# Kernel tuning notes

Measured on AMD Instinct MI355X. Metric: run time of the kernel, lower is better.

## Reference

```python
import jax, jax.numpy as jnp
import numpy as np

EMBED_DIM = 2048
NUM_HEADS = 16
HEAD_DIM = EMBED_DIM // NUM_HEADS
ROPE_BASE = 10000.0


def setup_inputs() -> dict:
    key = jax.random.key(0)
    ks = jax.random.split(key, 5)
    s = 1.0 / np.sqrt(EMBED_DIM)
    return {
        "x": jax.random.normal(ks[0], (2, 2048, EMBED_DIM), dtype=jnp.float32),
        "Wq": jax.random.normal(ks[1], (EMBED_DIM, EMBED_DIM), dtype=jnp.float32) * s,
        "Wk": jax.random.normal(ks[2], (EMBED_DIM, EMBED_DIM), dtype=jnp.float32) * s,
        "Wv": jax.random.normal(ks[3], (EMBED_DIM, EMBED_DIM), dtype=jnp.float32) * s,
        "Wo": jax.random.normal(ks[4], (EMBED_DIM, EMBED_DIM), dtype=jnp.float32) * s,
    }


def _rope(x):
    # x: [b, h, s, d]; standard rotate-half RoPE
    b, h, s, d = x.shape
    inv_freq = 1.0 / (ROPE_BASE ** (jnp.arange(0, d, 2, dtype=jnp.float32) / d))
    ang = jnp.arange(s, dtype=jnp.float32)[:, None] * inv_freq[None, :]  # [s, d/2]
    cos = jnp.concatenate([jnp.cos(ang), jnp.cos(ang)], axis=-1)  # [s, d]
    sin = jnp.concatenate([jnp.sin(ang), jnp.sin(ang)], axis=-1)
    x1, x2 = x[..., : d // 2], x[..., d // 2 :]
    rot = jnp.concatenate([-x2, x1], axis=-1)
    return x * cos + rot * sin


def reference(x, Wq, Wk, Wv, Wo):
    b, s, e = x.shape
    h, d = NUM_HEADS, HEAD_DIM
    # projections (torch Linear: x @ W.T); W here stored so that y = x @ W
    q = (x @ Wq).reshape(b, s, h, d).transpose(0, 2, 1, 3)
    k = (x @ Wk).reshape(b, s, h, d).transpose(0, 2, 1, 3)
    v = (x @ Wv).reshape(b, s, h, d).transpose(0, 2, 1, 3)
    q = _rope(q)
    k = _rope(k)
    att = jnp.einsum("bhqd,bhkd->bhqk", q, k) / jnp.sqrt(jnp.float32(d))
    causal = jnp.tril(jnp.ones((s, s), dtype=bool))
    att = jnp.where(causal, att, -jnp.inf)
    att = jax.nn.softmax(att, axis=-1)
    out = jnp.einsum("bhqk,bhkd->bhqd", att, v)
    out = out.transpose(0, 2, 1, 3).reshape(b, s, e)
    return out @ Wo
```

## Files before the change

kernel.cpp:

```cpp
#include <hip/hip_runtime.h>
#include <stdint.h>

#define EDIM 2048
#define HH 16
#define DD 128
#define SS 2048
#define BB 2

typedef __attribute__((ext_vector_type(8))) __bf16 bf16x8;
typedef __attribute__((ext_vector_type(8))) unsigned short ushort8;
typedef __attribute__((ext_vector_type(4))) unsigned short ushort4v;
typedef __attribute__((ext_vector_type(4))) float f32x4;

__device__ __forceinline__ unsigned short f2b(float f) {
    union { float f; unsigned int u; } v; v.f = f;
    unsigned int u = v.u;
    unsigned int r = (u + 0x7fffu + ((u >> 16) & 1u)) >> 16;
    return (unsigned short)r;
}
__device__ __forceinline__ float b2f(unsigned short h) {
    union { unsigned int u; float f; } v; v.u = ((unsigned int)h) << 16;
    return v.f;
}
__device__ __forceinline__ bf16x8 lds8(const unsigned short* p) {
    return __builtin_bit_cast(bf16x8, *(const ushort8*)p);
}
__device__ __forceinline__ void gl_lds16(const unsigned short* g, unsigned short* l) {
    __builtin_amdgcn_global_load_lds(
        (const __attribute__((address_space(1))) void*)(const void*)g,
        (__attribute__((address_space(3))) void*)(void*)l, 16, 0, 0);
}


__global__ __launch_bounds__(256) void k_cvt_x(const float4* __restrict__ x,
                                               ushort4v* __restrict__ xb) {
    size_t i = (size_t)blockIdx.x * 256 + threadIdx.x;
    float4 v = x[i];
    ushort4v o;
    o.x = f2b(v.x); o.y = f2b(v.y); o.z = f2b(v.z); o.w = f2b(v.w);
    xb[i] = o;
}

__global__ __launch_bounds__(256) void k_trans(const float* __restrict__ W0,
                                               const float* __restrict__ W1,
                                               const float* __restrict__ W2,
                                               const float* __restrict__ W3,
                                               unsigned short* __restrict__ Wt) {
    const float* W = (blockIdx.z == 0) ? W0 : (blockIdx.z == 1) ? W1
                     : (blockIdx.z == 2) ? W2 : W3;
    unsigned short* out = Wt + (size_t)blockIdx.z * EDIM * EDIM;
    __shared__ float t[64][65];
    int r0 = blockIdx.y * 64, c0 = blockIdx.x * 64;
#pragma unroll
    for (int i = 0; i < 16; ++i) {
        int e = threadIdx.x + i * 256; int r = e >> 6, c = e & 63;
        t[r][c] = W[(size_t)(r0 + r) * EDIM + c0 + c];
    }
    __syncthreads();
#pragma unroll
    for (int i = 0; i < 16; ++i) {
        int e = threadIdx.x + i * 256; int r = e >> 6, c = e & 63;
        out[(size_t)(c0 + r) * EDIM + r0 + c] = f2b(t[c][r]);
    }
}


__device__ __forceinline__ void gemm_core(const unsigned short* __restrict__ A,
                                          const unsigned short* __restrict__ Bt,
                                          int K, size_t m0, size_t n0,
                                          unsigned short* As, unsigned short* Bs,
                                          f32x4 acc[4][4], int wave, int lane) {
    const int wm = wave >> 1, wn = wave & 1;
    const int lg = lane >> 4, lr = lane & 15;
    for (int kt = 0; kt < K; kt += 32) {
#pragma unroll
        for (int j = 0; j < 2; ++j) {
            const int cb = j * 256 + wave * 64;
            const int c  = cb + lane;
            gl_lds16(A  + (m0 + (size_t)(c >> 2)) * K + kt + (c & 3) * 8, As + cb * 8);
            gl_lds16(Bt + (n0 + (size_t)(c >> 2)) * K + kt + (c & 3) * 8, Bs + cb * 8);
        }
        __syncthreads();
        bf16x8 af[4], bg[4];
#pragma unroll
        for (int i = 0; i < 4; ++i) {
            af[i] = lds8(As + (wm * 64 + i * 16 + lr) * 32 + lg * 8);
            bg[i] = lds8(Bs + (wn * 64 + i * 16 + lr) * 32 + lg * 8);
        }
#pragma unroll
        for (int i = 0; i < 4; ++i)
#pragma unroll
            for (int j = 0; j < 4; ++j)
                acc[i][j] = __builtin_amdgcn_mfma_f32_16x16x32_bf16(af[i], bg[j], acc[i][j], 0, 0, 0);
        __syncthreads();
    }
}

__global__ __launch_bounds__(256) void k_gemm_qkv(const unsigned short* __restrict__ xb,
                                                  const unsigned short* __restrict__ Wt,
                                                  unsigned short* __restrict__ Qd,
                                                  unsigned short* __restrict__ Kd,
                                                  unsigned short* __restrict__ Vtd) {
    __shared__ alignas(16) unsigned short As[128 * 32];
    __shared__ alignas(16) unsigned short Bs[128 * 32];
    const int tid = threadIdx.x, wave = tid >> 6, lane = tid & 63;
    const int wsel = blockIdx.y >> 4;
    const size_t m0 = (size_t)blockIdx.x * 128;
    const size_t n0 = (size_t)(blockIdx.y & 15) * 128;
    const unsigned short* Bw = Wt + (size_t)wsel * EDIM * EDIM;
    f32x4 acc[4][4] = {};
    gemm_core(xb, Bw, EDIM, m0, n0, As, Bs, acc, wave, lane);
    const int wm = wave >> 1, wn = wave & 1, lg = lane >> 4, lr = lane & 15;
    if (wsel < 2) {
        unsigned short* dst = wsel ? Kd : Qd;
#pragma unroll
        for (int i = 0; i < 4; ++i)
#pragma unroll
            for (int j = 0; j < 4; ++j)
#pragma unroll
                for (int r = 0; r < 4; ++r) {
                    int row = (int)m0 + wm * 64 + i * 16 + lg * 4 + r;
                    int e   = (int)n0 + wn * 64 + j * 16 + lr;
                    int b = row >> 11, s = row & (SS - 1);
                    int h = e >> 7,  d = e & (DD - 1);
                    dst[(((size_t)(b * HH + h)) * SS + s) * DD + d] = f2b(acc[i][j][r]);
                }
    } else {
#pragma unroll
        for (int i = 0; i < 4; ++i)
#pragma unroll
            for (int j = 0; j < 4; ++j) {
                int row0 = (int)m0 + wm * 64 + i * 16 + lg * 4;
                int e    = (int)n0 + wn * 64 + j * 16 + lr;
                int b = row0 >> 11, s0 = row0 & (SS - 1);
                int h = e >> 7, d = e & (DD - 1);
                ushort4v pk;
                pk.x = f2b(acc[i][j][0]); pk.y = f2b(acc[i][j][1]);
                pk.z = f2b(acc[i][j][2]); pk.w = f2b(acc[i][j][3]);
                *(ushort4v*)(Vtd + (((size_t)(b * HH + h)) * DD + d) * SS + s0) = pk;
            }
    }
}

__global__ __launch_bounds__(256) void k_gemm_out(const unsigned short* __restrict__ Ob,
                                                  const unsigned short* __restrict__ Wto,
                                                  float* __restrict__ y) {
    __shared__ alignas(16) unsigned short As[128 * 32];
    __shared__ alignas(16) unsigned short Bs[128 * 32];
    const int tid = threadIdx.x, wave = tid >> 6, lane = tid & 63;
    const size_t m0 = (size_t)blockIdx.x * 128;
    const size_t n0 = (size_t)blockIdx.y * 128;
    f32x4 acc[4][4] = {};
    gemm_core(Ob, Wto, EDIM, m0, n0, As, Bs, acc, wave, lane);
    const int wm = wave >> 1, wn = wave & 1, lg = lane >> 4, lr = lane & 15;
#pragma unroll
    for (int i = 0; i < 4; ++i)
#pragma unroll
        for (int j = 0; j < 4; ++j)
#pragma unroll
            for (int r = 0; r < 4; ++r) {
                size_t row = m0 + wm * 64 + i * 16 + lg * 4 + r;
                size_t col = n0 + wn * 64 + j * 16 + lr;
                y[row * EDIM + col] = acc[i][j][r];
            }
}


__global__ __launch_bounds__(256) void k_rope(unsigned short* __restrict__ Q,
                                              unsigned short* __restrict__ K) {
    int idx = blockIdx.x * 256 + threadIdx.x;
    int i  = idx & 63;
    int s  = (idx >> 6) & (SS - 1);
    int bh = idx >> 17;
    size_t base = ((size_t)bh * SS + s) * DD;
    float inv = __expf(-0.14391156608f * (float)i);
    float ang = (float)s * inv;
    float sn, cs; sincosf(ang, &sn, &cs);
    const float qs = 0.08838834764831845f;
    float q1 = b2f(Q[base + i]), q2 = b2f(Q[base + 64 + i]);
    float k1 = b2f(K[base + i]), k2 = b2f(K[base + 64 + i]);
    Q[base + i]      = f2b((q1 * cs - q2 * sn) * qs);
    Q[base + 64 + i] = f2b((q2 * cs + q1 * sn) * qs);
    K[base + i]      = f2b(k1 * cs - k2 * sn);
    K[base + 64 + i] = f2b(k2 * cs + k1 * sn);
}


__global__ __launch_bounds__(256) void k_attn(const unsigned short* __restrict__ Q,
                                              const unsigned short* __restrict__ Kg,
                                              const unsigned short* __restrict__ Vt,
                                              unsigned short* __restrict__ Ob) {
    __shared__ alignas(16) unsigned short Ks[64 * 136];
    __shared__ alignas(16) unsigned short Vs[128 * 72];
    __shared__ alignas(16) unsigned short Ps[64 * 72];
    const int tid = threadIdx.x, wave = tid >> 6, lane = tid & 63;
    const int lg = lane >> 4, lr = lane & 15;
    const int bh = blockIdx.y;
    const int q0 = ((int)gridDim.x - 1 - (int)blockIdx.x) * 64;
    const size_t qkb = (size_t)bh * SS * DD;
    const size_t vbb = (size_t)bh * DD * SS;

    bf16x8 qf[4];
    {
        const unsigned short* qp = Q + qkb + (size_t)(q0 + wave * 16 + lr) * DD + lg * 8;
#pragma unroll
        for (int kk = 0; kk < 4; ++kk)
            qf[kk] = __builtin_bit_cast(bf16x8, *(const ushort8*)(qp + kk * 32));
    }
    f32x4 o[8] = {};
    float mrow[4], lrow[4];
#pragma unroll
    for (int r = 0; r < 4; ++r) { mrow[r] = -1e30f; lrow[r] = 0.f; }

    const int nt = q0 / 64 + 1;
    for (int t = 0; t < nt; ++t) {
        const int kv0 = t * 64;
        __syncthreads();
#pragma unroll
        for (int it = 0; it < 4; ++it) {
            int c = tid + it * 256;
            { int r = c >> 4, off = (c & 15) * 8;
              *(ushort8*)(Ks + r * 136 + off) =
                  *(const ushort8*)(Kg + qkb + (size_t)(kv0 + r) * DD + off); }
            { int dr = c >> 3, off = (c & 7) * 8;
              *(ushort8*)(Vs + dr * 72 + off) =
                  *(const ushort8*)(Vt + vbb + (size_t)dr * SS + kv0 + off); }
        }
        __syncthreads();

        f32x4 sa[4] = {};
#pragma unroll
        for (int nf = 0; nf < 4; ++nf)
#pragma unroll
            for (int kk = 0; kk < 4; ++kk) {
                bf16x8 kb = lds8(Ks + (nf * 16 + lr) * 136 + kk * 32 + lg * 8);
                sa[nf] = __builtin_amdgcn_mfma_f32_16x16x32_bf16(qf[kk], kb, sa[nf], 0, 0, 0);
            }
        if (t == nt - 1) {
#pragma unroll
            for (int nf = 0; nf < 4; ++nf)
#pragma unroll
                for (int r = 0; r < 4; ++r) {
                    int col = nf * 16 + lr, rw = wave * 16 + lg * 4 + r;
                    if (col > rw) sa[nf][r] = -__builtin_inff();
                }
        }
        float corr[4];
#pragma unroll
        for (int r = 0; r < 4; ++r) {
            float tm = fmaxf(fmaxf(sa[0][r], sa[1][r]), fmaxf(sa[2][r], sa[3][r]));
#pragma unroll
            for (int mm = 1; mm < 16; mm <<= 1) tm = fmaxf(tm, __shfl_xor(tm, mm));
            float mn = fmaxf(mrow[r], tm);
            corr[r] = __expf(mrow[r] - mn);
            mrow[r] = mn;
        }
#pragma unroll
        for (int nf = 0; nf < 4; ++nf)
#pragma unroll
            for (int r = 0; r < 4; ++r) {
                float p = __expf(sa[nf][r] - mrow[r]);
                sa[nf][r] = p;
                Ps[(wave * 16 + lg * 4 + r) * 72 + nf * 16 + lr] = f2b(p);
            }
#pragma unroll
        for (int r = 0; r < 4; ++r) {
            float sm = sa[0][r] + sa[1][r] + sa[2][r] + sa[3][r];
#pragma unroll
            for (int mm = 1; mm < 16; mm <<= 1) sm += __shfl_xor(sm, mm);
            lrow[r] = lrow[r] * corr[r] + sm;
        }
#pragma unroll
        for (int nf = 0; nf < 8; ++nf)
#pragma unroll
            for (int r = 0; r < 4; ++r) o[nf][r] *= corr[r];

        bf16x8 pa0 = lds8(Ps + (wave * 16 + lr) * 72 + lg * 8);
        bf16x8 pa1 = lds8(Ps + (wave * 16 + lr) * 72 + 32 + lg * 8);
#pragma unroll
        for (int nf = 0; nf < 8; ++nf) {
            bf16x8 v0 = lds8(Vs + (nf * 16 + lr) * 72 + lg * 8);
            bf16x8 v1 = lds8(Vs + (nf * 16 + lr) * 72 + 32 + lg * 8);
            o[nf] = __builtin_amdgcn_mfma_f32_16x16x32_bf16(pa0, v0, o[nf], 0, 0, 0);
            o[nf] = __builtin_amdgcn_mfma_f32_16x16x32_bf16(pa1, v1, o[nf], 0, 0, 0);
        }
    }
    const int b = bh >> 4, h = bh & 15;
#pragma unroll
    for (int nf = 0; nf < 8; ++nf)
#pragma unroll
        for (int r = 0; r < 4; ++r) {
            int s = q0 + wave * 16 + lg * 4 + r;
            int e = h * DD + nf * 16 + lr;
            Ob[((size_t)b * SS + s) * EDIM + e] = f2b(o[nf][r] / lrow[r]);
        }
}


extern "C" void kernel_launch(void* const* d_in, const int* in_sizes, int n_in,
                              void* d_out, int out_size, void* d_ws, size_t ws_size,
                              hipStream_t stream) {
    const float* x  = (const float*)d_in[0];
    const float* Wq = (const float*)d_in[1];
    const float* Wk = (const float*)d_in[2];
    const float* Wv = (const float*)d_in[3];
    const float* Wo = (const float*)d_in[4];
    float* y = (float*)d_out;
    char* ws = (char*)d_ws;
    unsigned short* xb  = (unsigned short*)(ws);
    unsigned short* Wt  = (unsigned short*)(ws + (size_t)16777216);
    unsigned short* Qd  = (unsigned short*)(ws + (size_t)50331648);
    unsigned short* Kd  = (unsigned short*)(ws + (size_t)67108864);
    unsigned short* Vtd = (unsigned short*)(ws + (size_t)83886080);
    unsigned short* Ob  = (unsigned short*)(ws + (size_t)100663296);

    hipLaunchKernelGGL(k_cvt_x, dim3(8192), dim3(256), 0, stream, (const float4*)x, (ushort4v*)xb);
    hipLaunchKernelGGL(k_trans, dim3(32, 32, 4), dim3(256), 0, stream, Wq, Wk, Wv, Wo, Wt);
    hipLaunchKernelGGL(k_gemm_qkv, dim3(32, 48), dim3(256), 0, stream, xb, Wt, Qd, Kd, Vtd);
    hipLaunchKernelGGL(k_rope, dim3(16384), dim3(256), 0, stream, Qd, Kd);
    hipLaunchKernelGGL(k_attn, dim3(32, 32), dim3(256), 0, stream, Qd, Kd, Vtd, Ob);
    hipLaunchKernelGGL(k_gemm_out, dim3(32, 16), dim3(256), 0, stream,
                       Ob, Wt + (size_t)3 * EDIM * EDIM, y);
}
```

Baseline: 509.1 us.

## Pair causal query tiles per block and restructure attention softmax pipeline

Each attention block now handles two query tiles (tp and 31-tp), which balances causal work and lets both share each staged K/V tile, halving the grid. K/V global loads are register-prefetched one tile ahead, the softmax uses exp2 with log2e folded into the Q scale, and rescaling is skipped unless the row max grows by more than 8. The row sum comes from an extra ones-row in V computed by MFMA instead of shuffles, and s_setprio is raised around MFMA sections. In exchange register pressure and LDS use rise, and the grid has fewer blocks.

```diff
diff --git a/kernel.cpp b/kernel.cpp
--- a/kernel.cpp
+++ b/kernel.cpp
@@ -176,7 +176,7 @@
     float inv = __expf(-0.14391156608f * (float)i);
     float ang = (float)s * inv;
     float sn, cs; sincosf(ang, &sn, &cs);
-    const float qs = 0.08838834764831845f;
+    const float qs = 0.08838834764831845f * 1.44269504088896340736f;
     float q1 = b2f(Q[base + i]), q2 = b2f(Q[base + 64 + i]);
     float k1 = b2f(K[base + i]), k2 = b2f(K[base + 64 + i]);
     Q[base + i]      = f2b((q1 * cs - q2 * sn) * qs);
@@ -186,113 +186,146 @@
 }
 
 
+__device__ __forceinline__ void attn_tile(const unsigned short* Ks, const unsigned short* Vs,
+                                          unsigned short* Ps, const bf16x8 qf[4],
+                                          f32x4 o[9], float mrow[4], bool maskdiag,
+                                          int wave, int lg, int lr) {
+    f32x4 sa[4] = {};
+    __builtin_amdgcn_s_setprio(1);
+#pragma unroll
+    for (int nf = 0; nf < 4; ++nf)
+#pragma unroll
+        for (int kk = 0; kk < 4; ++kk) {
+            bf16x8 kb = lds8(Ks + (nf * 16 + lr) * 136 + kk * 32 + lg * 8);
+            sa[nf] = __builtin_amdgcn_mfma_f32_16x16x32_bf16(qf[kk], kb, sa[nf], 0, 0, 0);
+        }
+    __builtin_amdgcn_s_setprio(0);
+    if (maskdiag) {
+#pragma unroll
+        for (int nf = 0; nf < 4; ++nf)
+#pragma unroll
+            for (int r = 0; r < 4; ++r) {
+                int col = nf * 16 + lr, rw = wave * 16 + lg * 4 + r;
+                if (col > rw) sa[nf][r] = -__builtin_inff();
+            }
+    }
+    float tm[4]; bool need = false;
+#pragma unroll
+    for (int r = 0; r < 4; ++r) {
+        float t = fmaxf(fmaxf(sa[0][r], sa[1][r]), fmaxf(sa[2][r], sa[3][r]));
+#pragma unroll
+        for (int mm = 1; mm < 16; mm <<= 1) t = fmaxf(t, __shfl_xor(t, mm));
+        tm[r] = t;
+        need = need || (t > mrow[r] + 8.0f);
+    }
+    if (__any(need)) {
+        float corr[4];
+#pragma unroll
+        for (int r = 0; r < 4; ++r) {
+            float mn = fmaxf(mrow[r], tm[r]);
+            corr[r] = exp2f(mrow[r] - mn);
+            mrow[r] = mn;
+        }
+#pragma unroll
+        for (int nf = 0; nf < 9; ++nf)
+#pragma unroll
+            for (int r = 0; r < 4; ++r) o[nf][r] *= corr[r];
+    }
+#pragma unroll
+    for (int nf = 0; nf < 4; ++nf)
+#pragma unroll
+        for (int r = 0; r < 4; ++r)
+            Ps[(wave * 16 + lg * 4 + r) * 72 + nf * 16 + lr] = f2b(exp2f(sa[nf][r] - mrow[r]));
+    bf16x8 pa0 = lds8(Ps + (wave * 16 + lr) * 72 + lg * 8);
+    bf16x8 pa1 = lds8(Ps + (wave * 16 + lr) * 72 + 32 + lg * 8);
+    __builtin_amdgcn_s_setprio(1);
+#pragma unroll
+    for (int nf = 0; nf < 9; ++nf) {
+        bf16x8 v0 = lds8(Vs + (nf * 16 + lr) * 72 + lg * 8);
+        bf16x8 v1 = lds8(Vs + (nf * 16 + lr) * 72 + 32 + lg * 8);
+        o[nf] = __builtin_amdgcn_mfma_f32_16x16x32_bf16(pa0, v0, o[nf], 0, 0, 0);
+        o[nf] = __builtin_amdgcn_mfma_f32_16x16x32_bf16(pa1, v1, o[nf], 0, 0, 0);
+    }
+    __builtin_amdgcn_s_setprio(0);
+}
+
 __global__ __launch_bounds__(256) void k_attn(const unsigned short* __restrict__ Q,
                                               const unsigned short* __restrict__ Kg,
                                               const unsigned short* __restrict__ Vt,
                                               unsigned short* __restrict__ Ob) {
     __shared__ alignas(16) unsigned short Ks[64 * 136];
-    __shared__ alignas(16) unsigned short Vs[128 * 72];
+    __shared__ alignas(16) unsigned short Vs[144 * 72];
     __shared__ alignas(16) unsigned short Ps[64 * 72];
     const int tid = threadIdx.x, wave = tid >> 6, lane = tid & 63;
     const int lg = lane >> 4, lr = lane & 15;
     const int bh = blockIdx.y;
-    const int q0 = ((int)gridDim.x - 1 - (int)blockIdx.x) * 64;
+    const int tp = blockIdx.x;
+    const int qa0 = tp * 64, qb0 = (31 - tp) * 64;
+    const int nta = tp + 1, ntb = 32 - tp;
     const size_t qkb = (size_t)bh * SS * DD;
     const size_t vbb = (size_t)bh * DD * SS;
 
-    bf16x8 qf[4];
     {
-        const unsigned short* qp = Q + qkb + (size_t)(q0 + wave * 16 + lr) * DD + lg * 8;
-#pragma unroll
-        for (int kk = 0; kk < 4; ++kk)
-            qf[kk] = __builtin_bit_cast(bf16x8, *(const ushort8*)(qp + kk * 32));
-    }
-    f32x4 o[8] = {};
-    float mrow[4], lrow[4];
-#pragma unroll
-    for (int r = 0; r < 4; ++r) { mrow[r] = -1e30f; lrow[r] = 0.f; }
-
-    const int nt = q0 / 64 + 1;
-    for (int t = 0; t < nt; ++t) {
-        const int kv0 = t * 64;
+        ushort4v one4; one4.x = 0x3F80; one4.y = 0x3F80; one4.z = 0x3F80; one4.w = 0x3F80;
+        *(ushort4v*)(Vs + (128 + (tid >> 4)) * 72 + (tid & 15) * 4) = one4;
+    }
+
+    bf16x8 qfA[4], qfB[4];
+    {
+        const unsigned short* qpA = Q + qkb + (size_t)(qa0 + wave * 16 + lr) * DD + lg * 8;
+        const unsigned short* qpB = Q + qkb + (size_t)(qb0 + wave * 16 + lr) * DD + lg * 8;
+#pragma unroll
+        for (int kk = 0; kk < 4; ++kk) {
+            qfA[kk] = __builtin_bit_cast(bf16x8, *(const ushort8*)(qpA + kk * 32));
+            qfB[kk] = __builtin_bit_cast(bf16x8, *(const ushort8*)(qpB + kk * 32));
+        }
+    }
+    f32x4 oA[9] = {}, oB[9] = {};
+    float mA[4], mB[4];
+#pragma unroll
+    for (int r = 0; r < 4; ++r) { mA[r] = -3e38f; mB[r] = -3e38f; }
+
+    ushort8 kr[4], vr[4];
+#pragma unroll
+    for (int i = 0; i < 4; ++i) {
+        int c = tid + i * 256;
+        kr[i] = *(const ushort8*)(Kg + qkb + (size_t)(c >> 4) * DD + (c & 15) * 8);
+        vr[i] = *(const ushort8*)(Vt + vbb + (size_t)(c >> 3) * SS + (c & 7) * 8);
+    }
+
+    for (int t = 0; t < ntb; ++t) {
         __syncthreads();
 #pragma unroll
-        for (int it = 0; it < 4; ++it) {
-            int c = tid + it * 256;
-            { int r = c >> 4, off = (c & 15) * 8;
-              *(ushort8*)(Ks + r * 136 + off) =
-                  *(const ushort8*)(Kg + qkb + (size_t)(kv0 + r) * DD + off); }
-            { int dr = c >> 3, off = (c & 7) * 8;
-              *(ushort8*)(Vs + dr * 72 + off) =
-                  *(const ushort8*)(Vt + vbb + (size_t)dr * SS + kv0 + off); }
+        for (int i = 0; i < 4; ++i) {
+            int c = tid + i * 256;
+            *(ushort8*)(Ks + (c >> 4) * 136 + (c & 15) * 8) = kr[i];
+            *(ushort8*)(Vs + (c >> 3) * 72 + (c & 7) * 8) = vr[i];
         }
         __syncthreads();
-
-        f32x4 sa[4] = {};
-#pragma unroll
-        for (int nf = 0; nf < 4; ++nf)
-#pragma unroll
-            for (int kk = 0; kk < 4; ++kk) {
-                bf16x8 kb = lds8(Ks + (nf * 16 + lr) * 136 + kk * 32 + lg * 8);
-                sa[nf] = __builtin_amdgcn_mfma_f32_16x16x32_bf16(qf[kk], kb, sa[nf], 0, 0, 0);
+        if (t + 1 < ntb) {
+            int kv0 = (t + 1) * 64;
+#pragma unroll
+            for (int i = 0; i < 4; ++i) {
+                int c = tid + i * 256;
+                kr[i] = *(const ushort8*)(Kg + qkb + (size_t)(kv0 + (c >> 4)) * DD + (c & 15) * 8);
+                vr[i] = *(const ushort8*)(Vt + vbb + (size_t)(c >> 3) * SS + kv0 + (c & 7) * 8);
             }
-        if (t == nt - 1) {
-#pragma unroll
-            for (int nf = 0; nf < 4; ++nf)
-#pragma unroll
-                for (int r = 0; r < 4; ++r) {
-                    int col = nf * 16 + lr, rw = wave * 16 + lg * 4 + r;
-                    if (col > rw) sa[nf][r] = -__builtin_inff();
-                }
-        }
-        float corr[4];
+        }
+        attn_tile(Ks, Vs, Ps, qfB, oB, mB, t == ntb - 1, wave, lg, lr);
+        if (t < nta)
+            attn_tile(Ks, Vs, Ps, qfA, oA, mA, t == nta - 1, wave, lg, lr);
+    }
+
+    const int b = bh >> 4, h = bh & 15;
+#pragma unroll
+    for (int nf = 0; nf < 8; ++nf)
 #pragma unroll
         for (int r = 0; r < 4; ++r) {
-            float tm = fmaxf(fmaxf(sa[0][r], sa[1][r]), fmaxf(sa[2][r], sa[3][r]));
-#pragma unroll
-            for (int mm = 1; mm < 16; mm <<= 1) tm = fmaxf(tm, __shfl_xor(tm, mm));
-            float mn = fmaxf(mrow[r], tm);
-            corr[r] = __expf(mrow[r] - mn);
-            mrow[r] = mn;
-        }
-#pragma unroll
-        for (int nf = 0; nf < 4; ++nf)
-#pragma unroll
-            for (int r = 0; r < 4; ++r) {
-                float p = __expf(sa[nf][r] - mrow[r]);
-                sa[nf][r] = p;
-                Ps[(wave * 16 + lg * 4 + r) * 72 + nf * 16 + lr] = f2b(p);
-            }
-#pragma unroll
-        for (int r = 0; r < 4; ++r) {
-            float sm = sa[0][r] + sa[1][r] + sa[2][r] + sa[3][r];
-#pragma unroll
-            for (int mm = 1; mm < 16; mm <<= 1) sm += __shfl_xor(sm, mm);
-            lrow[r] = lrow[r] * corr[r] + sm;
-        }
-#pragma unroll
-        for (int nf = 0; nf < 8; ++nf)
-#pragma unroll
-            for (int r = 0; r < 4; ++r) o[nf][r] *= corr[r];
-
-        bf16x8 pa0 = lds8(Ps + (wave * 16 + lr) * 72 + lg * 8);
-        bf16x8 pa1 = lds8(Ps + (wave * 16 + lr) * 72 + 32 + lg * 8);
-#pragma unroll
-        for (int nf = 0; nf < 8; ++nf) {
-            bf16x8 v0 = lds8(Vs + (nf * 16 + lr) * 72 + lg * 8);
-            bf16x8 v1 = lds8(Vs + (nf * 16 + lr) * 72 + 32 + lg * 8);
-            o[nf] = __builtin_amdgcn_mfma_f32_16x16x32_bf16(pa0, v0, o[nf], 0, 0, 0);
-            o[nf] = __builtin_amdgcn_mfma_f32_16x16x32_bf16(pa1, v1, o[nf], 0, 0, 0);
-        }
-    }
-    const int b = bh >> 4, h = bh & 15;
-#pragma unroll
-    for (int nf = 0; nf < 8; ++nf)
-#pragma unroll
-        for (int r = 0; r < 4; ++r) {
-            int s = q0 + wave * 16 + lg * 4 + r;
+            int sA = qa0 + wave * 16 + lg * 4 + r;
+            int sB = qb0 + wave * 16 + lg * 4 + r;
             int e = h * DD + nf * 16 + lr;
-            Ob[((size_t)b * SS + s) * EDIM + e] = f2b(o[nf][r] / lrow[r]);
+            Ob[((size_t)b * SS + sA) * EDIM + e] = f2b(oA[nf][r] / oA[8][r]);
+            Ob[((size_t)b * SS + sB) * EDIM + e] = f2b(oB[nf][r] / oB[8][r]);
         }
 }
 
@@ -318,7 +351,7 @@
     hipLaunchKernelGGL(k_trans, dim3(32, 32, 4), dim3(256), 0, stream, Wq, Wk, Wv, Wo, Wt);
     hipLaunchKernelGGL(k_gemm_qkv, dim3(32, 48), dim3(256), 0, stream, xb, Wt, Qd, Kd, Vtd);
     hipLaunchKernelGGL(k_rope, dim3(16384), dim3(256), 0, stream, Qd, Kd);
-    hipLaunchKernelGGL(k_attn, dim3(32, 32), dim3(256), 0, stream, Qd, Kd, Vtd, Ob);
+    hipLaunchKernelGGL(k_attn, dim3(16, 32), dim3(256), 0, stream, Qd, Kd, Vtd, Ob);
     hipLaunchKernelGGL(k_gemm_out, dim3(32, 16), dim3(256), 0, stream,
                        Ob, Wt + (size_t)3 * EDIM * EDIM, y);
 }
```

Result: faster. 497.9 us (-2.2%).
